# Performance work log

Measured on AMD Instinct MI355X. Metric: run time of the kernel, lower is better.

## Reference

```python
import jax, jax.numpy as jnp
import numpy as np
from jax.ops import segment_sum


def gcn_conv(x, src, dst, W, b, num_nodes):
    # PyG GCNConv: x' = D^{-1/2} (A + I) D^{-1/2} (x @ W) + b
    loops = jnp.arange(num_nodes, dtype=src.dtype)
    s = jnp.concatenate([src, loops])  # source of each edge (incl. self-loops)
    d = jnp.concatenate([dst, loops])  # destination of each edge
    ones = jnp.ones(s.shape[0], dtype=x.dtype)
    deg = segment_sum(ones, d, num_segments=num_nodes)  # in-degree incl. self-loop
    dinv = jnp.where(deg > 0, jax.lax.rsqrt(deg), 0.0)
    norm = dinv[s] * dinv[d]  # [E+N]
    h = x @ W  # [N, C_out] dense transform first (C_out <= C_in typical)
    msg = h[s] * norm[:, None]  # gather + scale  [E+N, C_out]
    out = segment_sum(msg, d, num_segments=num_nodes)  # scatter-add
    return out + b


def setup_inputs() -> dict:
    key = jax.random.key(0)
    k1, k2, k3, k4 = jax.random.split(key, 4)
    N, E = 100000, 1600000
    C_in, C_out = 64, 32
    C_hid = 2 * C_out
    x = jax.random.normal(k1, (N, C_in), dtype=jnp.float32)
    edge_index = jax.random.randint(k2, (2, E), 0, N, dtype=jnp.int64)
    # Glorot-style init for the linear weights, zero bias (PyG defaults)
    W1 = jax.random.normal(k3, (C_in, C_hid), dtype=jnp.float32) * (1.0 / np.sqrt(C_in))
    b1 = jnp.zeros((C_hid,), dtype=jnp.float32)
    W2 = jax.random.normal(k4, (C_hid, C_out), dtype=jnp.float32) * (1.0 / np.sqrt(C_hid))
    b2 = jnp.zeros((C_out,), dtype=jnp.float32)
    return {"x": x, "edge_index": edge_index, "num_nodes": N,
            "W1": W1, "b1": b1, "W2": W2, "b2": b2}


def reference(x, edge_index, num_nodes, W1, b1, W2, b2):
    src, dst = edge_index[0], edge_index[1]
    h = gcn_conv(x, src, dst, W1, b1, num_nodes)
    h = jax.nn.relu(h)
    out = gcn_conv(h, src, dst, W2, b2, num_nodes)
    return out
```

## Files before the change

kernel.cpp:

```cpp
#include <hip/hip_runtime.h>


constexpr int CAP = 8192;
constexpr int NBMAX = 512;

__device__ inline unsigned short f2bf(float f) {
    unsigned u = __float_as_uint(f);
    u += 0x7fff + ((u >> 16) & 1);
    return (unsigned short)(u >> 16);
}
__device__ inline float bflo(unsigned u) { return __uint_as_float(u << 16); }
__device__ inline float bfhi(unsigned u) { return __uint_as_float(u & 0xffff0000u); }

__device__ inline void acc8(float* acc, uint4 u) {
    acc[0] += bflo(u.x); acc[1] += bfhi(u.x);
    acc[2] += bflo(u.y); acc[3] += bfhi(u.y);
    acc[4] += bflo(u.z); acc[5] += bfhi(u.z);
    acc[6] += bflo(u.w); acc[7] += bfhi(u.w);
}

template <int STRIDE>
__device__ inline void walk_pipe(const uint4* __restrict__ hs, const int* __restrict__ col,
                                 int q, int es, int ee, float* acc) {
    int e = es;
    if (e + 8 <= ee) {
        uint4 b[8];
        int s[8];
#pragma unroll
        for (int j = 0; j < 8; ++j) s[j] = col[e + j];
#pragma unroll
        for (int j = 0; j < 8; ++j) b[j] = hs[(size_t)s[j] * STRIDE + q];
        e += 8;
        while (e + 8 <= ee) {
            uint4 nb[8];
            int ns[8];
#pragma unroll
            for (int j = 0; j < 8; ++j) ns[j] = col[e + j];
#pragma unroll
            for (int j = 0; j < 8; ++j) nb[j] = hs[(size_t)ns[j] * STRIDE + q];
#pragma unroll
            for (int j = 0; j < 8; ++j) acc8(acc, b[j]);
#pragma unroll
            for (int j = 0; j < 8; ++j) b[j] = nb[j];
            e += 8;
        }
#pragma unroll
        for (int j = 0; j < 8; ++j) acc8(acc, b[j]);
    }
    if (e + 4 <= ee) {
        int s0 = col[e], s1 = col[e + 1], s2 = col[e + 2], s3 = col[e + 3];
        uint4 b0 = hs[(size_t)s0 * STRIDE + q];
        uint4 b1 = hs[(size_t)s1 * STRIDE + q];
        uint4 b2 = hs[(size_t)s2 * STRIDE + q];
        uint4 b3 = hs[(size_t)s3 * STRIDE + q];
        acc8(acc, b0); acc8(acc, b1); acc8(acc, b2); acc8(acc, b3);
        e += 4;
    }
    for (; e < ee; ++e) acc8(acc, hs[(size_t)col[e] * STRIDE + q]);
}

__global__ __launch_bounds__(256) void p1_bin(const int* __restrict__ src,
                                              const int* __restrict__ dst,
                                              int* __restrict__ bucketCursor,
                                              unsigned* __restrict__ staging, int E, int NB) {
    __shared__ int cnt[NBMAX];
    __shared__ int cur[NBMAX];
    int tid = threadIdx.x;
    for (int i = tid; i < NB; i += 256) cnt[i] = 0;
    __syncthreads();
    int e0 = blockIdx.x * 4096;
#pragma unroll
    for (int k = 0; k < 16; ++k) {
        int e = e0 + k * 256 + tid;
        if (e < E) atomicAdd(&cnt[dst[e] >> 8], 1);
    }
    __syncthreads();
    for (int i = tid; i < NB; i += 256) {
        int c = cnt[i];
        cur[i] = c ? atomicAdd(&bucketCursor[i], c) : 0;
    }
    __syncthreads();
#pragma unroll
    for (int k = 0; k < 16; ++k) {
        int e = e0 + k * 256 + tid;
        if (e < E) {
            int d = dst[e];
            int b = d >> 8;
            int slot = atomicAdd(&cur[b], 1);
            staging[(size_t)b * CAP + slot] = ((unsigned)src[e] << 8) | (unsigned)(d & 255);
        }
    }
}

__global__ __launch_bounds__(256) void p2_csr(const unsigned* __restrict__ staging,
                                              const int* __restrict__ bucketCursor,
                                              int* __restrict__ rp, int* __restrict__ col,
                                              float* __restrict__ dinv, int N, int E, int NB) {
    __shared__ int sb[NBMAX];
    __shared__ int deg[256];
    __shared__ int scn[256];
    __shared__ int cur[256];
    int b = blockIdx.x;
    int tid = threadIdx.x;
    int i1 = tid, i2 = tid + 256;
    sb[i1] = (i1 < NB) ? bucketCursor[i1] : 0;
    sb[i2] = (i2 < NB) ? bucketCursor[i2] : 0;
    deg[tid] = 0;
    __syncthreads();
    for (int off = 1; off < NBMAX; off <<= 1) {
        int a = (i1 >= off) ? sb[i1 - off] : 0;
        int c = (i2 >= off) ? sb[i2 - off] : 0;
        __syncthreads();
        sb[i1] += a;
        sb[i2] += c;
        __syncthreads();
    }
    int base = (b == 0) ? 0 : sb[b - 1];
    int size = sb[b] - base;
    if (b == 0 && tid == 0) rp[N] = E;
    const unsigned* st = staging + (size_t)b * CAP;
    for (int i = tid; i < size; i += 256) atomicAdd(&deg[st[i] & 255u], 1);
    __syncthreads();
    int g = b * 256 + tid;
    int d = deg[tid];
    if (g < N) dinv[g] = rsqrtf((float)(d + 1));
    scn[tid] = d;
    __syncthreads();
    for (int off = 1; off < 256; off <<= 1) {
        int t = (tid >= off) ? scn[tid - off] : 0;
        __syncthreads();
        scn[tid] += t;
        __syncthreads();
    }
    int excl = scn[tid] - d;
    if (g < N) rp[g] = base + excl;
    cur[tid] = excl;
    __syncthreads();
    for (int i = tid; i < size; i += 256) {
        unsigned pk = st[i];
        int pos = atomicAdd(&cur[pk & 255u], 1);
        col[base + pos] = (int)(pk >> 8);
    }
}

__global__ __launch_bounds__(256) void gemm1(const float* __restrict__ X,
                                             const float* __restrict__ W,
                                             const float* __restrict__ dinv,
                                             unsigned short* __restrict__ Hout, int N) {
    constexpr int XS = 65;
    __shared__ float Xs[128 * XS];
    __shared__ float Ws[64 * 64];
    int tid = threadIdx.x;
    int rowBase = blockIdx.x * 128;
    const float4* Wv = (const float4*)W;
    float4* Wsv = (float4*)Ws;
    for (int i = tid; i < 64 * 64 / 4; i += 256) Wsv[i] = Wv[i];
    const float4* Xv = (const float4*)X;
    for (int v = tid; v < 128 * 16; v += 256) {
        int r = v >> 4, j = v & 15;
        int gr = rowBase + r;
        float4 t = make_float4(0.f, 0.f, 0.f, 0.f);
        if (gr < N) t = Xv[(size_t)gr * 16 + j];
        int b = r * XS + j * 4;
        Xs[b] = t.x;
        Xs[b + 1] = t.y;
        Xs[b + 2] = t.z;
        Xs[b + 3] = t.w;
    }
    __syncthreads();
    int cg = tid % 8, rg = tid / 8;
    int c0 = cg * 8, r0 = rg * 4;
    float acc[4][8];
#pragma unroll
    for (int i = 0; i < 4; ++i)
#pragma unroll
        for (int j = 0; j < 8; ++j) acc[i][j] = 0.f;
#pragma unroll 8
    for (int k = 0; k < 64; ++k) {
        float4 w0 = *(const float4*)&Ws[k * 64 + c0];
        float4 w1 = *(const float4*)&Ws[k * 64 + c0 + 4];
        float xr[4];
#pragma unroll
        for (int i = 0; i < 4; ++i) xr[i] = Xs[(r0 + i) * XS + k];
#pragma unroll
        for (int i = 0; i < 4; ++i) {
            acc[i][0] = fmaf(xr[i], w0.x, acc[i][0]);
            acc[i][1] = fmaf(xr[i], w0.y, acc[i][1]);
            acc[i][2] = fmaf(xr[i], w0.z, acc[i][2]);
            acc[i][3] = fmaf(xr[i], w0.w, acc[i][3]);
            acc[i][4] = fmaf(xr[i], w1.x, acc[i][4]);
            acc[i][5] = fmaf(xr[i], w1.y, acc[i][5]);
            acc[i][6] = fmaf(xr[i], w1.z, acc[i][6]);
            acc[i][7] = fmaf(xr[i], w1.w, acc[i][7]);
        }
    }
#pragma unroll
    for (int i = 0; i < 4; ++i) {
        int row = rowBase + r0 + i;
        if (row >= N) continue;
        float dn = dinv[row];
        unsigned pk[4];
#pragma unroll
        for (int j = 0; j < 4; ++j) {
            unsigned lo = f2bf(acc[i][2 * j] * dn);
            unsigned hi = f2bf(acc[i][2 * j + 1] * dn);
            pk[j] = lo | (hi << 16);
        }
        *(uint4*)(Hout + (size_t)row * 64 + c0) = make_uint4(pk[0], pk[1], pk[2], pk[3]);
    }
}

__global__ __launch_bounds__(256) void agg1_gemm2(
    const uint4* __restrict__ hs1, const float* __restrict__ dinv, const int* __restrict__ rp,
    const int* __restrict__ col, const float* __restrict__ b1, const float* __restrict__ W2,
    unsigned short* __restrict__ h2, int N) {
    constexpr int RS = 68;
    constexpr int NPB = 16;
    __shared__ float rows[NPB * RS];
    __shared__ float Ws2[64 * 32];
    int tid = threadIdx.x;
    const float4* W2v = (const float4*)W2;
    float4* Ws2v = (float4*)Ws2;
    for (int i = tid; i < 64 * 32 / 4; i += 256) Ws2v[i] = W2v[i];

    int r = tid >> 4;
    int t16 = tid & 15;
    int sg = t16 >> 3;
    int q = t16 & 7;
    int node = blockIdx.x * NPB + r;
    float dn = 0.f;
    float acc[8];
#pragma unroll
    for (int j = 0; j < 8; ++j) acc[j] = 0.f;
    if (node < N) {
        dn = dinv[node];
        if (sg == 0) acc8(acc, hs1[(size_t)node * 8 + q]);
        int e0 = rp[node], e1 = rp[node + 1];
        int mid = (e0 + e1 + 1) >> 1;
        walk_pipe<8>(hs1, col, q, sg ? mid : e0, sg ? e1 : mid, acc);
    }
#pragma unroll
    for (int j = 0; j < 8; ++j) acc[j] += __shfl_xor(acc[j], 8, 64);
    if (node < N && sg == 0) {
        const float4* bv = (const float4*)b1;
        float4 bb0 = bv[q * 2], bb1 = bv[q * 2 + 1];
        float* myrow = &rows[r * RS + q * 8];
        *(float4*)myrow =
            make_float4(fmaxf(fmaf(acc[0], dn, bb0.x), 0.f), fmaxf(fmaf(acc[1], dn, bb0.y), 0.f),
                        fmaxf(fmaf(acc[2], dn, bb0.z), 0.f), fmaxf(fmaf(acc[3], dn, bb0.w), 0.f));
        *(float4*)(myrow + 4) =
            make_float4(fmaxf(fmaf(acc[4], dn, bb1.x), 0.f), fmaxf(fmaf(acc[5], dn, bb1.y), 0.f),
                        fmaxf(fmaf(acc[6], dn, bb1.z), 0.f), fmaxf(fmaf(acc[7], dn, bb1.w), 0.f));
    }
    __syncthreads();

    if (node >= N) return;
    int c0 = t16 * 2;
    float a0 = 0.f, a1 = 0.f;
    const float* row = &rows[r * RS];
#pragma unroll
    for (int k4 = 0; k4 < 16; ++k4) {
        float4 xq = *(const float4*)&row[k4 * 4];
#pragma unroll
        for (int kk = 0; kk < 4; ++kk) {
            float xv = (&xq.x)[kk];
            float2 w = *(const float2*)&Ws2[(k4 * 4 + kk) * 32 + c0];
            a0 = fmaf(xv, w.x, a0);
            a1 = fmaf(xv, w.y, a1);
        }
    }
    unsigned pk = (unsigned)f2bf(a0 * dn) | ((unsigned)f2bf(a1 * dn) << 16);
    *(unsigned*)(h2 + (size_t)node * 32 + c0) = pk;
}

__global__ __launch_bounds__(256) void agg2(const uint4* __restrict__ hs2,
                                            const float* __restrict__ dinv,
                                            const int* __restrict__ rp,
                                            const int* __restrict__ col,
                                            const float* __restrict__ bias,
                                            float* __restrict__ out, int N) {
    int tid = blockIdx.x * blockDim.x + threadIdx.x;
    int node = tid >> 3;
    int t8 = tid & 7;
    int sg = t8 >> 2, q = t8 & 3;
    if (node >= N) return;
    float acc[8];
#pragma unroll
    for (int j = 0; j < 8; ++j) acc[j] = 0.f;
    if (sg == 0) acc8(acc, hs2[(size_t)node * 4 + q]);
    int e0 = rp[node], e1 = rp[node + 1];
    int mid = (e0 + e1 + 1) >> 1;
    walk_pipe<4>(hs2, col, q, sg ? mid : e0, sg ? e1 : mid, acc);
#pragma unroll
    for (int j = 0; j < 8; ++j) acc[j] += __shfl_xor(acc[j], 4, 64);
    if (sg) return;
    float dn = dinv[node];
    const float4* bv = (const float4*)bias;
    float4 b0 = bv[q * 2], b1 = bv[q * 2 + 1];
    float4* ov = (float4*)(out + (size_t)node * 32 + q * 8);
    ov[0] = make_float4(fmaf(acc[0], dn, b0.x), fmaf(acc[1], dn, b0.y), fmaf(acc[2], dn, b0.z),
                        fmaf(acc[3], dn, b0.w));
    ov[1] = make_float4(fmaf(acc[4], dn, b1.x), fmaf(acc[5], dn, b1.y), fmaf(acc[6], dn, b1.z),
                        fmaf(acc[7], dn, b1.w));
}

extern "C" void kernel_launch(void* const* d_in, const int* in_sizes, int n_in,
                              void* d_out, int out_size, void* d_ws, size_t ws_size,
                              hipStream_t stream) {
    const float* x = (const float*)d_in[0];
    const int* ei = (const int*)d_in[1];
    const float* W1 = (const float*)d_in[3];
    const float* b1 = (const float*)d_in[4];
    const float* W2 = (const float*)d_in[5];
    const float* b2 = (const float*)d_in[6];

    constexpr int CIN = 64, CHID = 64;
    const int N = in_sizes[0] / CIN;
    const int E = in_sizes[1] / 2;
    const int* src = ei;
    const int* dst = ei + E;
    const int NB = (N + 255) >> 8;

    char* p = (char*)d_ws;
    auto carve = [&](size_t bytes) -> void* {
        void* q = (void*)p;
        p += (bytes + 255) & ~(size_t)255;
        return q;
    };
    int* bucketCursor = (int*)carve((size_t)NB * 4);
    int* rp = (int*)carve((size_t)(N + 1) * 4);
    int* col = (int*)carve((size_t)E * 4);
    float* dinv = (float*)carve((size_t)N * 4);
    unsigned* staging = (unsigned*)carve((size_t)NB * CAP * 4);
    unsigned short* h1 = (unsigned short*)carve((size_t)N * CHID * 2);
    unsigned short* h2 = (unsigned short*)staging;

    hipMemsetAsync(bucketCursor, 0, (size_t)NB * 4, stream);
    p1_bin<<<(E + 4095) / 4096, 256, 0, stream>>>(src, dst, bucketCursor, staging, E, NB);
    p2_csr<<<NB, 256, 0, stream>>>(staging, bucketCursor, rp, col, dinv, N, E, NB);

    gemm1<<<(N + 127) / 128, 256, 0, stream>>>(x, W1, dinv, h1, N);
    agg1_gemm2<<<(N + 15) / 16, 256, 0, stream>>>((const uint4*)h1, dinv, rp, col, b1, W2, h2, N);
    agg2<<<((size_t)N * 8 + 255) / 256, 256, 0, stream>>>((const uint4*)h2, dinv, rp, col, b2,
                                                          (float*)d_out, N);
}
```

Baseline: 225.7 us.

## Aggregate raw features before W1 and fuse both GEMMs into aggregation kernel

Uses linearity, A(XW) = (AX)W, to aggregate the dinv-scaled bf16 input features first and apply W1 afterwards, so the separate gemm1 kernel disappears. The scaling and bf16 conversion of x moves into the CSR-build kernel, and the aggregation kernel then runs W1, bias, ReLU and W2 from shared memory. The deep 8-wide prefetch gather loop is also swapped for a simpler 4-wide loop. This saves one kernel launch and the write and read of h1. In exchange, the aggregation kernel holds more shared memory, adds block syncs, and does the 64x64 matmul per node inside it.

```diff
diff --git a/kernel.cpp b/kernel.cpp
--- a/kernel.cpp
+++ b/kernel.cpp
@@ -20,41 +20,16 @@
 }
 
 template <int STRIDE>
-__device__ inline void walk_pipe(const uint4* __restrict__ hs, const int* __restrict__ col,
-                                 int q, int es, int ee, float* acc) {
+__device__ inline void walk4(const uint4* __restrict__ hs, const int* __restrict__ col, int q,
+                             int es, int ee, float* acc) {
     int e = es;
-    if (e + 8 <= ee) {
-        uint4 b[8];
-        int s[8];
-#pragma unroll
-        for (int j = 0; j < 8; ++j) s[j] = col[e + j];
-#pragma unroll
-        for (int j = 0; j < 8; ++j) b[j] = hs[(size_t)s[j] * STRIDE + q];
-        e += 8;
-        while (e + 8 <= ee) {
-            uint4 nb[8];
-            int ns[8];
-#pragma unroll
-            for (int j = 0; j < 8; ++j) ns[j] = col[e + j];
-#pragma unroll
-            for (int j = 0; j < 8; ++j) nb[j] = hs[(size_t)ns[j] * STRIDE + q];
-#pragma unroll
-            for (int j = 0; j < 8; ++j) acc8(acc, b[j]);
-#pragma unroll
-            for (int j = 0; j < 8; ++j) b[j] = nb[j];
-            e += 8;
-        }
-#pragma unroll
-        for (int j = 0; j < 8; ++j) acc8(acc, b[j]);
-    }
-    if (e + 4 <= ee) {
+    for (; e + 4 <= ee; e += 4) {
         int s0 = col[e], s1 = col[e + 1], s2 = col[e + 2], s3 = col[e + 3];
-        uint4 b0 = hs[(size_t)s0 * STRIDE + q];
-        uint4 b1 = hs[(size_t)s1 * STRIDE + q];
-        uint4 b2 = hs[(size_t)s2 * STRIDE + q];
-        uint4 b3 = hs[(size_t)s3 * STRIDE + q];
-        acc8(acc, b0); acc8(acc, b1); acc8(acc, b2); acc8(acc, b3);
-        e += 4;
+        uint4 u0 = hs[(size_t)s0 * STRIDE + q];
+        uint4 u1 = hs[(size_t)s1 * STRIDE + q];
+        uint4 u2 = hs[(size_t)s2 * STRIDE + q];
+        uint4 u3 = hs[(size_t)s3 * STRIDE + q];
+        acc8(acc, u0); acc8(acc, u1); acc8(acc, u2); acc8(acc, u3);
     }
     for (; e < ee; ++e) acc8(acc, hs[(size_t)col[e] * STRIDE + q]);
 }
@@ -94,12 +69,16 @@
 
 __global__ __launch_bounds__(256) void p2_csr(const unsigned* __restrict__ staging,
                                               const int* __restrict__ bucketCursor,
+                                              const float* __restrict__ x,
                                               int* __restrict__ rp, int* __restrict__ col,
-                                              float* __restrict__ dinv, int N, int E, int NB) {
+                                              float* __restrict__ dinv,
+                                              unsigned short* __restrict__ xs,
+                                              int N, int E, int NB) {
     __shared__ int sb[NBMAX];
     __shared__ int deg[256];
     __shared__ int scn[256];
     __shared__ int cur[256];
+    __shared__ float dinvs[256];
     int b = blockIdx.x;
     int tid = threadIdx.x;
     int i1 = tid, i2 = tid + 256;
@@ -123,7 +102,9 @@
     __syncthreads();
     int g = b * 256 + tid;
     int d = deg[tid];
-    if (g < N) dinv[g] = rsqrtf((float)(d + 1));
+    float dn = rsqrtf((float)(d + 1));
+    dinvs[tid] = dn;
+    if (g < N) dinv[g] = dn;
     scn[tid] = d;
     __syncthreads();
     for (int off = 1; off < 256; off <<= 1) {
@@ -141,87 +122,41 @@
         int pos = atomicAdd(&cur[pk & 255u], 1);
         col[base + pos] = (int)(pk >> 8);
     }
-}
-
-__global__ __launch_bounds__(256) void gemm1(const float* __restrict__ X,
-                                             const float* __restrict__ W,
-                                             const float* __restrict__ dinv,
-                                             unsigned short* __restrict__ Hout, int N) {
-    constexpr int XS = 65;
-    __shared__ float Xs[128 * XS];
-    __shared__ float Ws[64 * 64];
-    int tid = threadIdx.x;
-    int rowBase = blockIdx.x * 128;
-    const float4* Wv = (const float4*)W;
-    float4* Wsv = (float4*)Ws;
-    for (int i = tid; i < 64 * 64 / 4; i += 256) Wsv[i] = Wv[i];
-    const float4* Xv = (const float4*)X;
-    for (int v = tid; v < 128 * 16; v += 256) {
+    const float4* Xv = (const float4*)x;
+    uint2* xsv = (uint2*)xs;
+    int rowBase = b * 256;
+    for (int v = tid; v < 256 * 16; v += 256) {
         int r = v >> 4, j = v & 15;
         int gr = rowBase + r;
-        float4 t = make_float4(0.f, 0.f, 0.f, 0.f);
-        if (gr < N) t = Xv[(size_t)gr * 16 + j];
-        int b = r * XS + j * 4;
-        Xs[b] = t.x;
-        Xs[b + 1] = t.y;
-        Xs[b + 2] = t.z;
-        Xs[b + 3] = t.w;
-    }
-    __syncthreads();
-    int cg = tid % 8, rg = tid / 8;
-    int c0 = cg * 8, r0 = rg * 4;
-    float acc[4][8];
-#pragma unroll
-    for (int i = 0; i < 4; ++i)
-#pragma unroll
-        for (int j = 0; j < 8; ++j) acc[i][j] = 0.f;
-#pragma unroll 8
-    for (int k = 0; k < 64; ++k) {
-        float4 w0 = *(const float4*)&Ws[k * 64 + c0];
-        float4 w1 = *(const float4*)&Ws[k * 64 + c0 + 4];
-        float xr[4];
-#pragma unroll
-        for (int i = 0; i < 4; ++i) xr[i] = Xs[(r0 + i) * XS + k];
-#pragma unroll
-        for (int i = 0; i < 4; ++i) {
-            acc[i][0] = fmaf(xr[i], w0.x, acc[i][0]);
-            acc[i][1] = fmaf(xr[i], w0.y, acc[i][1]);
-            acc[i][2] = fmaf(xr[i], w0.z, acc[i][2]);
-            acc[i][3] = fmaf(xr[i], w0.w, acc[i][3]);
-            acc[i][4] = fmaf(xr[i], w1.x, acc[i][4]);
-            acc[i][5] = fmaf(xr[i], w1.y, acc[i][5]);
-            acc[i][6] = fmaf(xr[i], w1.z, acc[i][6]);
-            acc[i][7] = fmaf(xr[i], w1.w, acc[i][7]);
+        if (gr < N) {
+            float4 t = Xv[(size_t)gr * 16 + j];
+            float s = dinvs[r];
+            uint2 pk;
+            pk.x = (unsigned)f2bf(t.x * s) | ((unsigned)f2bf(t.y * s) << 16);
+            pk.y = (unsigned)f2bf(t.z * s) | ((unsigned)f2bf(t.w * s) << 16);
+            xsv[(size_t)gr * 16 + j] = pk;
         }
     }
-#pragma unroll
-    for (int i = 0; i < 4; ++i) {
-        int row = rowBase + r0 + i;
-        if (row >= N) continue;
-        float dn = dinv[row];
-        unsigned pk[4];
-#pragma unroll
-        for (int j = 0; j < 4; ++j) {
-            unsigned lo = f2bf(acc[i][2 * j] * dn);
-            unsigned hi = f2bf(acc[i][2 * j + 1] * dn);
-            pk[j] = lo | (hi << 16);
-        }
-        *(uint4*)(Hout + (size_t)row * 64 + c0) = make_uint4(pk[0], pk[1], pk[2], pk[3]);
-    }
-}
-
-__global__ __launch_bounds__(256) void agg1_gemm2(
-    const uint4* __restrict__ hs1, const float* __restrict__ dinv, const int* __restrict__ rp,
-    const int* __restrict__ col, const float* __restrict__ b1, const float* __restrict__ W2,
-    unsigned short* __restrict__ h2, int N) {
+}
+
+__global__ __launch_bounds__(256) void agg_mlp(
+    const uint4* __restrict__ xs, const float* __restrict__ dinv, const int* __restrict__ rp,
+    const int* __restrict__ col, const float* __restrict__ b1, const float* __restrict__ W1,
+    const float* __restrict__ W2, unsigned short* __restrict__ h2, int N) {
     constexpr int RS = 68;
     constexpr int NPB = 16;
     __shared__ float rows[NPB * RS];
-    __shared__ float Ws2[64 * 32];
+    __shared__ float W1s[64 * 64];
+    __shared__ float W2s[64 * 32];
     int tid = threadIdx.x;
-    const float4* W2v = (const float4*)W2;
-    float4* Ws2v = (float4*)Ws2;
-    for (int i = tid; i < 64 * 32 / 4; i += 256) Ws2v[i] = W2v[i];
+    {
+        const float4* a = (const float4*)W1;
+        float4* d = (float4*)W1s;
+        for (int i = tid; i < 64 * 64 / 4; i += 256) d[i] = a[i];
+        const float4* a2 = (const float4*)W2;
+        float4* d2 = (float4*)W2s;
+        for (int i = tid; i < 64 * 32 / 4; i += 256) d2[i] = a2[i];
+    }
 
     int r = tid >> 4;
     int t16 = tid & 15;
@@ -234,43 +169,53 @@
     for (int j = 0; j < 8; ++j) acc[j] = 0.f;
     if (node < N) {
         dn = dinv[node];
-        if (sg == 0) acc8(acc, hs1[(size_t)node * 8 + q]);
+        if (sg == 0) acc8(acc, xs[(size_t)node * 8 + q]);
         int e0 = rp[node], e1 = rp[node + 1];
         int mid = (e0 + e1 + 1) >> 1;
-        walk_pipe<8>(hs1, col, q, sg ? mid : e0, sg ? e1 : mid, acc);
+        walk4<8>(xs, col, q, sg ? mid : e0, sg ? e1 : mid, acc);
     }
 #pragma unroll
     for (int j = 0; j < 8; ++j) acc[j] += __shfl_xor(acc[j], 8, 64);
     if (node < N && sg == 0) {
-        const float4* bv = (const float4*)b1;
-        float4 bb0 = bv[q * 2], bb1 = bv[q * 2 + 1];
         float* myrow = &rows[r * RS + q * 8];
-        *(float4*)myrow =
-            make_float4(fmaxf(fmaf(acc[0], dn, bb0.x), 0.f), fmaxf(fmaf(acc[1], dn, bb0.y), 0.f),
-                        fmaxf(fmaf(acc[2], dn, bb0.z), 0.f), fmaxf(fmaf(acc[3], dn, bb0.w), 0.f));
-        *(float4*)(myrow + 4) =
-            make_float4(fmaxf(fmaf(acc[4], dn, bb1.x), 0.f), fmaxf(fmaf(acc[5], dn, bb1.y), 0.f),
-                        fmaxf(fmaf(acc[6], dn, bb1.z), 0.f), fmaxf(fmaf(acc[7], dn, bb1.w), 0.f));
+        *(float4*)myrow = make_float4(acc[0] * dn, acc[1] * dn, acc[2] * dn, acc[3] * dn);
+        *(float4*)(myrow + 4) = make_float4(acc[4] * dn, acc[5] * dn, acc[6] * dn, acc[7] * dn);
     }
     __syncthreads();
 
     if (node >= N) return;
-    int c0 = t16 * 2;
-    float a0 = 0.f, a1 = 0.f;
+    int c0 = t16 * 4;
+    float a1[4] = {0.f, 0.f, 0.f, 0.f};
     const float* row = &rows[r * RS];
-#pragma unroll
-    for (int k4 = 0; k4 < 16; ++k4) {
-        float4 xq = *(const float4*)&row[k4 * 4];
-#pragma unroll
-        for (int kk = 0; kk < 4; ++kk) {
-            float xv = (&xq.x)[kk];
-            float2 w = *(const float2*)&Ws2[(k4 * 4 + kk) * 32 + c0];
-            a0 = fmaf(xv, w.x, a0);
-            a1 = fmaf(xv, w.y, a1);
-        }
-    }
-    unsigned pk = (unsigned)f2bf(a0 * dn) | ((unsigned)f2bf(a1 * dn) << 16);
-    *(unsigned*)(h2 + (size_t)node * 32 + c0) = pk;
+#pragma unroll 16
+    for (int k = 0; k < 64; ++k) {
+        float xv = row[k];
+        float4 w = *(const float4*)&W1s[k * 64 + c0];
+        a1[0] = fmaf(xv, w.x, a1[0]);
+        a1[1] = fmaf(xv, w.y, a1[1]);
+        a1[2] = fmaf(xv, w.z, a1[2]);
+        a1[3] = fmaf(xv, w.w, a1[3]);
+    }
+    float4 bb = *(const float4*)&b1[c0];
+    a1[0] = fmaxf(a1[0] + bb.x, 0.f);
+    a1[1] = fmaxf(a1[1] + bb.y, 0.f);
+    a1[2] = fmaxf(a1[2] + bb.z, 0.f);
+    a1[3] = fmaxf(a1[3] + bb.w, 0.f);
+    __syncthreads();
+    *(float4*)&rows[r * RS + c0] = make_float4(a1[0], a1[1], a1[2], a1[3]);
+    __syncthreads();
+
+    int c2 = t16 * 2;
+    float h0 = 0.f, h1v = 0.f;
+#pragma unroll 16
+    for (int k = 0; k < 64; ++k) {
+        float av = row[k];
+        float2 w = *(const float2*)&W2s[k * 32 + c2];
+        h0 = fmaf(av, w.x, h0);
+        h1v = fmaf(av, w.y, h1v);
+    }
+    unsigned pk = (unsigned)f2bf(h0 * dn) | ((unsigned)f2bf(h1v * dn) << 16);
+    *(unsigned*)(h2 + (size_t)node * 32 + c2) = pk;
 }
 
 __global__ __launch_bounds__(256) void agg2(const uint4* __restrict__ hs2,
@@ -290,7 +235,7 @@
     if (sg == 0) acc8(acc, hs2[(size_t)node * 4 + q]);
     int e0 = rp[node], e1 = rp[node + 1];
     int mid = (e0 + e1 + 1) >> 1;
-    walk_pipe<4>(hs2, col, q, sg ? mid : e0, sg ? e1 : mid, acc);
+    walk4<4>(hs2, col, q, sg ? mid : e0, sg ? e1 : mid, acc);
 #pragma unroll
     for (int j = 0; j < 8; ++j) acc[j] += __shfl_xor(acc[j], 4, 64);
     if (sg) return;
@@ -314,7 +259,7 @@
     const float* W2 = (const float*)d_in[5];
     const float* b2 = (const float*)d_in[6];
 
-    constexpr int CIN = 64, CHID = 64;
+    constexpr int CIN = 64;
     const int N = in_sizes[0] / CIN;
     const int E = in_sizes[1] / 2;
     const int* src = ei;
@@ -332,15 +277,15 @@
     int* col = (int*)carve((size_t)E * 4);
     float* dinv = (float*)carve((size_t)N * 4);
     unsigned* staging = (unsigned*)carve((size_t)NB * CAP * 4);
-    unsigned short* h1 = (unsigned short*)carve((size_t)N * CHID * 2);
+    unsigned short* xs = (unsigned short*)carve((size_t)N * CIN * 2);
     unsigned short* h2 = (unsigned short*)staging;
 
     hipMemsetAsync(bucketCursor, 0, (size_t)NB * 4, stream);
     p1_bin<<<(E + 4095) / 4096, 256, 0, stream>>>(src, dst, bucketCursor, staging, E, NB);
-    p2_csr<<<NB, 256, 0, stream>>>(staging, bucketCursor, rp, col, dinv, N, E, NB);
-
-    gemm1<<<(N + 127) / 128, 256, 0, stream>>>(x, W1, dinv, h1, N);
-    agg1_gemm2<<<(N + 15) / 16, 256, 0, stream>>>((const uint4*)h1, dinv, rp, col, b1, W2, h2, N);
+    p2_csr<<<NB, 256, 0, stream>>>(staging, bucketCursor, x, rp, col, dinv, xs, N, E, NB);
+
+    agg_mlp<<<(N + 15) / 16, 256, 0, stream>>>((const uint4*)xs, dinv, rp, col, b1, W1, W2, h2,
+                                               N);
     agg2<<<((size_t)N * 8 + 255) / 256, 256, 0, stream>>>((const uint4*)h2, dinv, rp, col, b2,
                                                           (float*)d_out, N);
 }
```

Measured after the change: 221.8 us. No clear change (-1.7%).
